# Performance work log

Measured on AMD Instinct MI355X. Metric: run time of the kernel, lower is better.

Reference implementation:

```python
import jax, jax.numpy as jnp
import numpy as np


def setup_inputs() -> dict:
    key = jax.random.key(0)
    k1, k2, k3 = jax.random.split(key, 3)
    x = jax.random.normal(k1, (8, 3, 256, 256), dtype=jnp.float32)
    conv_w = jax.random.normal(k2, (64, 3), dtype=jnp.float32)  # 1x1 conv weight [O, C]
    w = jax.random.normal(k3, (64, 8), dtype=jnp.float32)       # per-channel LBP weights
    return {"x": x, "conv_w": conv_w, "w": w}


def _heaviside(d):
    # torch.heaviside(d, 0.): 1 where d > 0, else 0 (including d == 0)
    return jnp.where(d > 0, jnp.ones((), d.dtype), jnp.zeros((), d.dtype))


def reference(x, conv_w, w):
    # 1x1 conv, no bias: [N,C,H,W] x [O,C] -> [N,O,H,W]
    y = jnp.einsum('nchw,oc->nohw', x, conv_w)
    c = y[:, :, 1:-1, 1:-1]  # center, [N,O,H-2,W-2]
    # 8 neighbor shifts in the original order
    shifts = [
        y[:, :, 0:-2, 0:-2], y[:, :, 0:-2, 1:-1], y[:, :, 0:-2, 2:],
        y[:, :, 1:-1, 0:-2], y[:, :, 2:, 0:-2], y[:, :, 2:, 1:-1],
        y[:, :, 2:, 2:],    y[:, :, 1:-1, 2:],
    ]
    act = jnp.stack([_heaviside(c - s) for s in shifts], axis=2)  # [N,O,8,H-2,W-2]
    # weighted reduction over the 8 directions with exp(w)
    x_cat = jnp.einsum('nolhw,ol->nohw', act, jnp.exp(w))
    padded = jnp.pad(x_cat, ((0, 0), (0, 0), (1, 1), (1, 1)))  # ZeroPad2d(1)
    # res=True: concat raw input along channels -> [N, 3+O, H, W]
    return jnp.concatenate([x, padded], axis=1)
```

## Files before the change

### kernel.cpp

```cpp
#include <hip/hip_runtime.h>


__device__ __forceinline__ float wave_shr1(float v) {
    return __int_as_float(
        __builtin_amdgcn_update_dpp(0, __float_as_int(v), 0x138, 0xf, 0xf, false));
}
__device__ __forceinline__ float wave_shl1(float v) {
    return __int_as_float(
        __builtin_amdgcn_update_dpp(0, __float_as_int(v), 0x130, 0xf, 0xf, false));
}

__global__ __launch_bounds__(256) void lbp_all(
    const float* __restrict__ x,
    const float* __restrict__ conv_w,
    const float* __restrict__ w,
    float* __restrict__ out)
{
#pragma clang fp contract(off)
    const int n     = blockIdx.z;
    const int og    = blockIdx.y;
    const int tid   = threadIdx.x;
    const int lane  = tid & 63;
    const int wv    = tid >> 6;
    const int col   = lane * 4;
    const int hrow0 = blockIdx.x * 8 + wv * 2;

    __shared__ float ews[128];
    if (tid < 128) ews[tid] = expf(w[og * 128 + tid]);

    const float* xn = x + (size_t)n * 3 * 65536;

    float4 xr[4][3];
    #pragma unroll
    for (int r = 0; r < 4; ++r) {
        int row = hrow0 - 1 + r;
        row = row < 0 ? 0 : (row > 255 ? 255 : row);
        #pragma unroll
        for (int ch = 0; ch < 3; ++ch)
            xr[r][ch] = *(const float4*)(xn + (ch * 256 + row) * 256 + col);
    }

    if (og == 0) {
        #pragma unroll
        for (int ch = 0; ch < 3; ++ch) {
            float* cp = out + ((((size_t)n * 67 + ch) * 256 + hrow0) * 256 + col);
            *(float4*)cp         = xr[1][ch];
            *(float4*)(cp + 256) = xr[2][ch];
        }
    }

    __syncthreads();

    float* obase = out + ((((size_t)n * 67 + 3 + og * 16) * 256 + hrow0) * 256 + col);

    #pragma unroll 4
    for (int oi = 0; oi < 16; ++oi) {
        const int o = og * 16 + oi;
        const float cw0 = conv_w[o * 3 + 0];
        const float cw1 = conv_w[o * 3 + 1];
        const float cw2 = conv_w[o * 3 + 2];

        float Y[4][6];
        #pragma unroll
        for (int r = 0; r < 4; ++r) {
            float4 yv;
            yv.x = xr[r][0].x * cw0 + xr[r][1].x * cw1 + xr[r][2].x * cw2;
            yv.y = xr[r][0].y * cw0 + xr[r][1].y * cw1 + xr[r][2].y * cw2;
            yv.z = xr[r][0].z * cw0 + xr[r][1].z * cw1 + xr[r][2].z * cw2;
            yv.w = xr[r][0].w * cw0 + xr[r][1].w * cw1 + xr[r][2].w * cw2;
            Y[r][1] = yv.x; Y[r][2] = yv.y; Y[r][3] = yv.z; Y[r][4] = yv.w;
            Y[r][0] = wave_shr1(yv.w);
            Y[r][5] = wave_shl1(yv.x);
        }

        const float e0 = ews[oi * 8 + 0], e1 = ews[oi * 8 + 1];
        const float e2 = ews[oi * 8 + 2], e3 = ews[oi * 8 + 3];
        const float e4 = ews[oi * 8 + 4], e5 = ews[oi * 8 + 5];
        const float e6 = ews[oi * 8 + 6], e7 = ews[oi * 8 + 7];

        #pragma unroll
        for (int k = 0; k < 2; ++k) {
            const int hrow = hrow0 + k;
            float res[4];
            if (hrow == 0 || hrow == 255) {
                res[0] = res[1] = res[2] = res[3] = 0.f;
            } else {
                const float* up  = Y[k];
                const float* mid = Y[k + 1];
                const float* dn  = Y[k + 2];
                #pragma unroll
                for (int j = 0; j < 4; ++j) {
                    const float c = mid[j + 1];
                    float acc;
                    acc  = (c > up [j    ]) ? e0 : 0.f;
                    acc += (c > up [j + 1]) ? e1 : 0.f;
                    acc += (c > up [j + 2]) ? e2 : 0.f;
                    acc += (c > mid[j    ]) ? e3 : 0.f;
                    acc += (c > dn [j    ]) ? e4 : 0.f;
                    acc += (c > dn [j + 1]) ? e5 : 0.f;
                    acc += (c > dn [j + 2]) ? e6 : 0.f;
                    acc += (c > mid[j + 2]) ? e7 : 0.f;
                    res[j] = acc;
                }
                if (lane == 0)  res[0] = 0.f;
                if (lane == 63) res[3] = 0.f;
            }
            *(float4*)(obase + (size_t)oi * 65536 + (size_t)k * 256) =
                make_float4(res[0], res[1], res[2], res[3]);
        }
    }
}

extern "C" void kernel_launch(void* const* d_in, const int* in_sizes, int n_in,
                              void* d_out, int out_size, void* d_ws, size_t ws_size,
                              hipStream_t stream) {
    const float* x      = (const float*)d_in[0];
    const float* conv_w = (const float*)d_in[1];
    const float* w      = (const float*)d_in[2];
    float* out          = (float*)d_out;

    dim3 grid(32, 4, 8);
    dim3 block(256);
    hipLaunchKernelGGL(lbp_all, grid, block, 0, stream, x, conv_w, w, out);
}
```

Before: 152.6 us.

## Stream rows per wave with rolling Y window, one output channel per wave

Remaps work so each wave owns one output channel and walks a 32-row strip. It keeps a rotating 4-row window of convolved rows and double-buffers the next input row's load. Redundant halo recomputation and the shared-memory exp table plus barrier are removed; exp weights become wave-uniform scalars. In exchange, input rows are re-read once per output channel, which relies on cache hits.

```diff
diff --git a/kernel.cpp b/kernel.cpp
--- a/kernel.cpp
+++ b/kernel.cpp
@@ -10,6 +10,62 @@
         __builtin_amdgcn_update_dpp(0, __float_as_int(v), 0x130, 0xf, 0xf, false));
 }
 
+#define LOAD3(BUF, ROW) do {                                                  \
+    int _r = (ROW); _r = _r < 0 ? 0 : (_r > 255 ? 255 : _r);                  \
+    const float* _p = xn + (size_t)_r * 256 + col;                            \
+    BUF[0] = *(const float4*)(_p);                                            \
+    BUF[1] = *(const float4*)(_p + 65536);                                    \
+    BUF[2] = *(const float4*)(_p + 131072);                                   \
+} while (0)
+
+#define CONV_ROW(BUF, SLOT) do {                                              \
+    float4 _y;                                                                \
+    _y.x = BUF[0].x * cw0 + BUF[1].x * cw1 + BUF[2].x * cw2;                  \
+    _y.y = BUF[0].y * cw0 + BUF[1].y * cw1 + BUF[2].y * cw2;                  \
+    _y.z = BUF[0].z * cw0 + BUF[1].z * cw1 + BUF[2].z * cw2;                  \
+    _y.w = BUF[0].w * cw0 + BUF[1].w * cw1 + BUF[2].w * cw2;                  \
+    Y[SLOT][1] = _y.x; Y[SLOT][2] = _y.y; Y[SLOT][3] = _y.z; Y[SLOT][4] = _y.w; \
+    Y[SLOT][0] = wave_shr1(_y.w);                                             \
+    Y[SLOT][5] = wave_shl1(_y.x);                                             \
+} while (0)
+
+#define COPYX(BUF, ROW) do {                                                  \
+    float* _cp = outn + (size_t)(ROW) * 256 + col;                            \
+    *(float4*)(_cp)          = BUF[0];                                        \
+    *(float4*)(_cp + 65536)  = BUF[1];                                        \
+    *(float4*)(_cp + 131072) = BUF[2];                                        \
+} while (0)
+
+#define EMIT(R, SU, SM, SD) do {                                              \
+    const int _row = (R);                                                     \
+    float res0, res1, res2, res3;                                             \
+    if (_row == 0 || _row == 255) {                                           \
+        res0 = res1 = res2 = res3 = 0.f;                                      \
+    } else {                                                                  \
+        res0 = res1 = res2 = res3 = 0.f;               \
+        float _r[4];                                                          \
+        _Pragma("unroll")                                                     \
+        for (int _j = 0; _j < 4; ++_j) {                                      \
+            const float _c = Y[SM][_j + 1];                                   \
+            float _a;                                                         \
+            _a  = (_c > Y[SU][_j    ]) ? e0 : 0.f;                            \
+            _a += (_c > Y[SU][_j + 1]) ? e1 : 0.f;                            \
+            _a += (_c > Y[SU][_j + 2]) ? e2 : 0.f;                            \
+            _a += (_c > Y[SM][_j    ]) ? e3 : 0.f;                            \
+            _a += (_c > Y[SD][_j    ]) ? e4 : 0.f;                            \
+            _a += (_c > Y[SD][_j + 1]) ? e5 : 0.f;                            \
+            _a += (_c > Y[SD][_j + 2]) ? e6 : 0.f;                            \
+            _a += (_c > Y[SM][_j + 2]) ? e7 : 0.f;                            \
+            _r[_j] = _a;                                                      \
+        }                                                                     \
+        res0 = _r[0]; res1 = _r[1]; res2 = _r[2]; res3 = _r[3];               \
+        if (lane == 0)  res0 = 0.f;                                           \
+        if (lane == 63) res3 = 0.f;                                           \
+    }                                                                         \
+    *(float4*)(ob + (size_t)_row * 256 + col) =                               \
+        make_float4(res0, res1, res2, res3);                                  \
+} while (0)
+
 __global__ __launch_bounds__(256) void lbp_all(
     const float* __restrict__ x,
     const float* __restrict__ conv_w,
@@ -17,98 +73,58 @@
     float* __restrict__ out)
 {
 #pragma clang fp contract(off)
-    const int n     = blockIdx.z;
-    const int og    = blockIdx.y;
-    const int tid   = threadIdx.x;
-    const int lane  = tid & 63;
-    const int wv    = tid >> 6;
-    const int col   = lane * 4;
-    const int hrow0 = blockIdx.x * 8 + wv * 2;
+    const int n    = blockIdx.z;
+    const int o    = blockIdx.y * 4 + (threadIdx.x >> 6);
+    const int lane = threadIdx.x & 63;
+    const int col  = lane * 4;
+    const int s0   = blockIdx.x * 32;
+    const bool copyx = (o == 0);
 
-    __shared__ float ews[128];
-    if (tid < 128) ews[tid] = expf(w[og * 128 + tid]);
+    const float cw0 = conv_w[o * 3 + 0];
+    const float cw1 = conv_w[o * 3 + 1];
+    const float cw2 = conv_w[o * 3 + 2];
 
-    const float* xn = x + (size_t)n * 3 * 65536;
+    const float e0 = __uint_as_float(__builtin_amdgcn_readfirstlane(__float_as_uint(expf(w[o * 8 + 0]))));
+    const float e1 = __uint_as_float(__builtin_amdgcn_readfirstlane(__float_as_uint(expf(w[o * 8 + 1]))));
+    const float e2 = __uint_as_float(__builtin_amdgcn_readfirstlane(__float_as_uint(expf(w[o * 8 + 2]))));
+    const float e3 = __uint_as_float(__builtin_amdgcn_readfirstlane(__float_as_uint(expf(w[o * 8 + 3]))));
+    const float e4 = __uint_as_float(__builtin_amdgcn_readfirstlane(__float_as_uint(expf(w[o * 8 + 4]))));
+    const float e5 = __uint_as_float(__builtin_amdgcn_readfirstlane(__float_as_uint(expf(w[o * 8 + 5]))));
+    const float e6 = __uint_as_float(__builtin_amdgcn_readfirstlane(__float_as_uint(expf(w[o * 8 + 6]))));
+    const float e7 = __uint_as_float(__builtin_amdgcn_readfirstlane(__float_as_uint(expf(w[o * 8 + 7]))));
 
-    float4 xr[4][3];
-    #pragma unroll
-    for (int r = 0; r < 4; ++r) {
-        int row = hrow0 - 1 + r;
-        row = row < 0 ? 0 : (row > 255 ? 255 : row);
-        #pragma unroll
-        for (int ch = 0; ch < 3; ++ch)
-            xr[r][ch] = *(const float4*)(xn + (ch * 256 + row) * 256 + col);
+    const float* xn   = x + (size_t)n * 3 * 65536;
+    float* outn       = out + (size_t)n * 67 * 65536;
+    float* ob         = outn + (size_t)(3 + o) * 65536;
+
+    float4 bA[3], bB[3];
+    float  Y[4][6];
+
+    LOAD3(bA, s0 - 1);
+    LOAD3(bB, s0);
+    CONV_ROW(bA, 3);
+    CONV_ROW(bB, 0);
+    if (copyx) COPYX(bB, s0);
+    LOAD3(bA, s0 + 1);
+
+#define STEP(JI) do {                                                         \
+    const int j = jo4 + (JI);                                                 \
+    if (((JI) & 1) == 0) {                                                    \
+        if (j < 31) LOAD3(bB, s0 + j + 2);                                    \
+        CONV_ROW(bA, ((JI) + 1) & 3);                                         \
+        if (copyx && j < 31) COPYX(bA, s0 + j + 1);                           \
+    } else {                                                                  \
+        if (j < 31) LOAD3(bA, s0 + j + 2);                                    \
+        CONV_ROW(bB, ((JI) + 1) & 3);                                         \
+        if (copyx && j < 31) COPYX(bB, s0 + j + 1);                           \
+    }                                                                         \
+    EMIT(s0 + j, ((JI) + 3) & 3, (JI) & 3, ((JI) + 1) & 3);                   \
+} while (0)
+
+    for (int jo4 = 0; jo4 < 32; jo4 += 4) {
+        STEP(0); STEP(1); STEP(2); STEP(3);
     }
-
-    if (og == 0) {
-        #pragma unroll
-        for (int ch = 0; ch < 3; ++ch) {
-            float* cp = out + ((((size_t)n * 67 + ch) * 256 + hrow0) * 256 + col);
-            *(float4*)cp         = xr[1][ch];
-            *(float4*)(cp + 256) = xr[2][ch];
-        }
-    }
-
-    __syncthreads();
-
-    float* obase = out + ((((size_t)n * 67 + 3 + og * 16) * 256 + hrow0) * 256 + col);
-
-    #pragma unroll 4
-    for (int oi = 0; oi < 16; ++oi) {
-        const int o = og * 16 + oi;
-        const float cw0 = conv_w[o * 3 + 0];
-        const float cw1 = conv_w[o * 3 + 1];
-        const float cw2 = conv_w[o * 3 + 2];
-
-        float Y[4][6];
-        #pragma unroll
-        for (int r = 0; r < 4; ++r) {
-            float4 yv;
-            yv.x = xr[r][0].x * cw0 + xr[r][1].x * cw1 + xr[r][2].x * cw2;
-            yv.y = xr[r][0].y * cw0 + xr[r][1].y * cw1 + xr[r][2].y * cw2;
-            yv.z = xr[r][0].z * cw0 + xr[r][1].z * cw1 + xr[r][2].z * cw2;
-            yv.w = xr[r][0].w * cw0 + xr[r][1].w * cw1 + xr[r][2].w * cw2;
-            Y[r][1] = yv.x; Y[r][2] = yv.y; Y[r][3] = yv.z; Y[r][4] = yv.w;
-            Y[r][0] = wave_shr1(yv.w);
-            Y[r][5] = wave_shl1(yv.x);
-        }
-
-        const float e0 = ews[oi * 8 + 0], e1 = ews[oi * 8 + 1];
-        const float e2 = ews[oi * 8 + 2], e3 = ews[oi * 8 + 3];
-        const float e4 = ews[oi * 8 + 4], e5 = ews[oi * 8 + 5];
-        const float e6 = ews[oi * 8 + 6], e7 = ews[oi * 8 + 7];
-
-        #pragma unroll
-        for (int k = 0; k < 2; ++k) {
-            const int hrow = hrow0 + k;
-            float res[4];
-            if (hrow == 0 || hrow == 255) {
-                res[0] = res[1] = res[2] = res[3] = 0.f;
-            } else {
-                const float* up  = Y[k];
-                const float* mid = Y[k + 1];
-                const float* dn  = Y[k + 2];
-                #pragma unroll
-                for (int j = 0; j < 4; ++j) {
-                    const float c = mid[j + 1];
-                    float acc;
-                    acc  = (c > up [j    ]) ? e0 : 0.f;
-                    acc += (c > up [j + 1]) ? e1 : 0.f;
-                    acc += (c > up [j + 2]) ? e2 : 0.f;
-                    acc += (c > mid[j    ]) ? e3 : 0.f;
-                    acc += (c > dn [j    ]) ? e4 : 0.f;
-                    acc += (c > dn [j + 1]) ? e5 : 0.f;
-                    acc += (c > dn [j + 2]) ? e6 : 0.f;
-                    acc += (c > mid[j + 2]) ? e7 : 0.f;
-                    res[j] = acc;
-                }
-                if (lane == 0)  res[0] = 0.f;
-                if (lane == 63) res[3] = 0.f;
-            }
-            *(float4*)(obase + (size_t)oi * 65536 + (size_t)k * 256) =
-                make_float4(res[0], res[1], res[2], res[3]);
-        }
-    }
+#undef STEP
 }
 
 extern "C" void kernel_launch(void* const* d_in, const int* in_sizes, int n_in,
@@ -119,7 +135,7 @@
     const float* w      = (const float*)d_in[2];
     float* out          = (float*)d_out;
 
-    dim3 grid(32, 4, 8);
+    dim3 grid(8, 16, 8);
     dim3 block(256);
     hipLaunchKernelGGL(lbp_all, grid, block, 0, stream, x, conv_w, w, out);
 }
```

Result: slower. 172.3 us (+12.9%).

## Stage input rows in shared memory and tree-reduce LBP direction sums

Applied to the files above, without the earlier changes.

Each block now loads its 10-row, 3-channel input tile cooperatively into shared memory once. Every output channel iteration then reads its four rows from there, instead of holding 48 input floats per thread in registers. The channel loop is no longer unrolled. The eight weighted comparisons are summed as a balanced tree instead of a serial chain, which shortens the dependency chain. The aim is lower register pressure and higher occupancy for this store-heavy kernel. In exchange the kernel pays about 30KB of LDS per block and repeated LDS reads, and the changed summation order can alter floating-point rounding.

```diff
diff --git a/kernel.cpp b/kernel.cpp
--- a/kernel.cpp
+++ b/kernel.cpp
@@ -17,66 +17,72 @@
     float* __restrict__ out)
 {
 #pragma clang fp contract(off)
-    const int n     = blockIdx.z;
-    const int og    = blockIdx.y;
-    const int tid   = threadIdx.x;
-    const int lane  = tid & 63;
-    const int wv    = tid >> 6;
-    const int col   = lane * 4;
-    const int hrow0 = blockIdx.x * 8 + wv * 2;
+    const int n    = blockIdx.z;
+    const int og   = blockIdx.y;
+    const int tid  = threadIdx.x;
+    const int lane = tid & 63;
+    const int wv   = tid >> 6;
+    const int col  = lane * 4;
+    const int R    = blockIdx.x * 8;
+    const int hrow0 = R + wv * 2;
 
+    __shared__ float xt[3][10][256];
     __shared__ float ews[128];
+
     if (tid < 128) ews[tid] = expf(w[og * 128 + tid]);
 
     const float* xn = x + (size_t)n * 3 * 65536;
 
-    float4 xr[4][3];
-    #pragma unroll
-    for (int r = 0; r < 4; ++r) {
-        int row = hrow0 - 1 + r;
-        row = row < 0 ? 0 : (row > 255 ? 255 : row);
-        #pragma unroll
-        for (int ch = 0; ch < 3; ++ch)
-            xr[r][ch] = *(const float4*)(xn + (ch * 256 + row) * 256 + col);
+    for (int f = tid; f < 1920; f += 256) {
+        const int ch = f / 640;
+        const int rr = (f - ch * 640) >> 6;
+        const int l4 = f & 63;
+        int gr = R - 1 + rr;
+        gr = gr < 0 ? 0 : (gr > 255 ? 255 : gr);
+        *(float4*)&xt[ch][rr][l4 * 4] =
+            *(const float4*)(xn + (size_t)ch * 65536 + (size_t)gr * 256 + l4 * 4);
     }
+    __syncthreads();
 
     if (og == 0) {
         #pragma unroll
         for (int ch = 0; ch < 3; ++ch) {
             float* cp = out + ((((size_t)n * 67 + ch) * 256 + hrow0) * 256 + col);
-            *(float4*)cp         = xr[1][ch];
-            *(float4*)(cp + 256) = xr[2][ch];
+            *(float4*)cp         = *(const float4*)&xt[ch][2 * wv + 1][col];
+            *(float4*)(cp + 256) = *(const float4*)&xt[ch][2 * wv + 2][col];
         }
     }
 
-    __syncthreads();
-
     float* obase = out + ((((size_t)n * 67 + 3 + og * 16) * 256 + hrow0) * 256 + col);
 
-    #pragma unroll 4
+    #pragma unroll 1
     for (int oi = 0; oi < 16; ++oi) {
         const int o = og * 16 + oi;
         const float cw0 = conv_w[o * 3 + 0];
         const float cw1 = conv_w[o * 3 + 1];
         const float cw2 = conv_w[o * 3 + 2];
 
+        const float e0 = ews[oi * 8 + 0], e1 = ews[oi * 8 + 1];
+        const float e2 = ews[oi * 8 + 2], e3 = ews[oi * 8 + 3];
+        const float e4 = ews[oi * 8 + 4], e5 = ews[oi * 8 + 5];
+        const float e6 = ews[oi * 8 + 6], e7 = ews[oi * 8 + 7];
+
         float Y[4][6];
         #pragma unroll
         for (int r = 0; r < 4; ++r) {
+            const int lr = 2 * wv + r;
+            const float4 a = *(const float4*)&xt[0][lr][col];
+            const float4 b = *(const float4*)&xt[1][lr][col];
+            const float4 c = *(const float4*)&xt[2][lr][col];
             float4 yv;
-            yv.x = xr[r][0].x * cw0 + xr[r][1].x * cw1 + xr[r][2].x * cw2;
-            yv.y = xr[r][0].y * cw0 + xr[r][1].y * cw1 + xr[r][2].y * cw2;
-            yv.z = xr[r][0].z * cw0 + xr[r][1].z * cw1 + xr[r][2].z * cw2;
-            yv.w = xr[r][0].w * cw0 + xr[r][1].w * cw1 + xr[r][2].w * cw2;
+            yv.x = a.x * cw0 + b.x * cw1 + c.x * cw2;
+            yv.y = a.y * cw0 + b.y * cw1 + c.y * cw2;
+            yv.z = a.z * cw0 + b.z * cw1 + c.z * cw2;
+            yv.w = a.w * cw0 + b.w * cw1 + c.w * cw2;
             Y[r][1] = yv.x; Y[r][2] = yv.y; Y[r][3] = yv.z; Y[r][4] = yv.w;
             Y[r][0] = wave_shr1(yv.w);
             Y[r][5] = wave_shl1(yv.x);
         }
-
-        const float e0 = ews[oi * 8 + 0], e1 = ews[oi * 8 + 1];
-        const float e2 = ews[oi * 8 + 2], e3 = ews[oi * 8 + 3];
-        const float e4 = ews[oi * 8 + 4], e5 = ews[oi * 8 + 5];
-        const float e6 = ews[oi * 8 + 6], e7 = ews[oi * 8 + 7];
 
         #pragma unroll
         for (int k = 0; k < 2; ++k) {
@@ -91,16 +97,15 @@
                 #pragma unroll
                 for (int j = 0; j < 4; ++j) {
                     const float c = mid[j + 1];
-                    float acc;
-                    acc  = (c > up [j    ]) ? e0 : 0.f;
-                    acc += (c > up [j + 1]) ? e1 : 0.f;
-                    acc += (c > up [j + 2]) ? e2 : 0.f;
-                    acc += (c > mid[j    ]) ? e3 : 0.f;
-                    acc += (c > dn [j    ]) ? e4 : 0.f;
-                    acc += (c > dn [j + 1]) ? e5 : 0.f;
-                    acc += (c > dn [j + 2]) ? e6 : 0.f;
-                    acc += (c > mid[j + 2]) ? e7 : 0.f;
-                    res[j] = acc;
+                    const float n0 = (c > up [j    ]) ? e0 : 0.f;
+                    const float n1 = (c > up [j + 1]) ? e1 : 0.f;
+                    const float n2 = (c > up [j + 2]) ? e2 : 0.f;
+                    const float n3 = (c > mid[j    ]) ? e3 : 0.f;
+                    const float n4 = (c > dn [j    ]) ? e4 : 0.f;
+                    const float n5 = (c > dn [j + 1]) ? e5 : 0.f;
+                    const float n6 = (c > dn [j + 2]) ? e6 : 0.f;
+                    const float n7 = (c > mid[j + 2]) ? e7 : 0.f;
+                    res[j] = ((n0 + n1) + (n2 + n3)) + ((n4 + n5) + (n6 + n7));
                 }
                 if (lane == 0)  res[0] = 0.f;
                 if (lane == 63) res[3] = 0.f;
```

Measured after the change: 154.2 us. No clear change (+1.0%).
